# Performance work log

Measured on AMD Instinct MI355X. Metric: run time of the kernel, lower is better.

The kernel has to match this reference:

```python
import jax, jax.numpy as jnp
import numpy as np

B, NA, NB, E = 2, 256, 256, 512
H1, H2 = 300, 100


def setup_inputs() -> dict:
    key = jax.random.key(0)
    ks = jax.random.split(key, 16)

    def n(k, shape, scale=1.0):
        return jax.random.normal(k, shape, dtype=jnp.float32) * scale

    z = lambda shape: jnp.zeros(shape, jnp.float32)
    return {
        "action_embedding": n(ks[0], (B, E, NA)),
        "anchor_embedding": n(ks[1], (B, E, NB)),
        "action_points": n(ks[2], (B, 3, NA)),
        "anchor_points": n(ks[3], (B, 3, NB)),
        # pairwise MLP kernel params: 2E -> 300 -> 100 -> 1
        "mlp_W1": n(ks[4], (2 * E, H1), (2 * E) ** -0.5),
        "mlp_b1": z((H1,)),
        "mlp_W2": n(ks[5], (H1, H2), H1 ** -0.5),
        "mlp_b2": z((H2,)),
        "mlp_W3": n(ks[6], (H2, 1), H2 ** -0.5),
        "mlp_b3": z((1,)),
        # PointNet [512,64,64,64,128,512] (1x1 convs) + Conv1d(512,1,bias=False)
        "pn_W0": n(ks[7], (64, 512), 512 ** -0.5),
        "pn_b0": z((64,)),
        "pn_W1": n(ks[8], (64, 64), 64 ** -0.5),
        "pn_b1": z((64,)),
        "pn_W2": n(ks[9], (64, 64), 64 ** -0.5),
        "pn_b2": z((64,)),
        "pn_W3": n(ks[10], (128, 64), 64 ** -0.5),
        "pn_b3": z((128,)),
        "pn_W4": n(ks[11], (512, 128), 128 ** -0.5),
        "pn_b4": z((512,)),
        "head_W": n(ks[12], (1, 512), 512 ** -0.5),
    }


def reference(action_embedding, anchor_embedding, action_points, anchor_points,
              mlp_W1, mlp_b1, mlp_W2, mlp_b2, mlp_W3, mlp_b3,
              pn_W0, pn_b0, pn_W1, pn_b1, pn_W2, pn_b2, pn_W3, pn_b3,
              pn_W4, pn_b4, head_W):
    P_A = action_points.transpose(0, 2, 1)      # (B, NA, 3)
    P_B = anchor_points.transpose(0, 2, 1)      # (B, NB, 3)
    Phi_A = action_embedding.transpose(0, 2, 1)  # (B, NA, E)
    Phi_B = anchor_embedding.transpose(0, 2, 1)  # (B, NB, E)
    Ed = Phi_A.shape[-1]

    # --- symmetric pairwise MLP kernel: softplus((mlp(cat(a,b)) + mlp(cat(b,a))) / 2) ---
    # First Linear layer is split so the O(NA*NB*2E) concat is never materialized:
    # cat(a,b) @ W1 == a @ W1[:E] + b @ W1[E:]
    W1a, W1b = mlp_W1[:Ed], mlp_W1[Ed:]

    def mlp_tail(h):  # h: (B, NA, NB, H1) pre-activation of layer 1
        h = jax.nn.relu(h)
        h = jax.nn.relu(h @ mlp_W2 + mlp_b2)
        return (h @ mlp_W3 + mlp_b3)[..., 0]  # (B, NA, NB)

    hA_a = Phi_A @ W1a  # (B, NA, H1)
    hA_b = Phi_A @ W1b
    hB_a = Phi_B @ W1a  # (B, NB, H1)
    hB_b = Phi_B @ W1b
    v1 = mlp_tail(hA_a[:, :, None, :] + hB_b[:, None, :, :] + mlp_b1)  # mlp(cat(x1,x2))
    v2 = mlp_tail(hB_a[:, None, :, :] + hA_b[:, :, None, :] + mlp_b1)  # mlp(cat(x2,x1))
    R_est = jax.nn.softplus((v1 + v2) * 0.5)  # (B, NA, NB) estimated distances

    # --- weighted multilateration (estimate_p), vectorized over (B, NA) ---
    # Linearized LS: ||p||^2 - 2 q_k^T p = r_k^2 - ||q_k||^2; subtract weighted means
    # to eliminate ||p||^2, then solve 3x3 weighted normal equations per action point.
    w = jnp.ones(P_B.shape[:2], R_est.dtype)            # (B, NB) uniform weights (last_attn=False)
    wsum = w.sum(-1, keepdims=True)                      # (B, 1)
    qbar = (w[..., None] * P_B).sum(1) / wsum            # (B, 3)
    bvec = (P_B ** 2).sum(-1)[:, None, :] - R_est ** 2   # (B, NA, NB)
    bbar = (w[:, None, :] * bvec).sum(-1) / wsum         # (B, NA)
    Amat = 2.0 * (P_B - qbar[:, None, :])                # (B, NB, 3)
    yvec = bvec - bbar[..., None]                        # (B, NA, NB)
    M = jnp.einsum('bki,bk,bkj->bij', Amat, w, Amat)     # (B, 3, 3)
    rhs = jnp.einsum('bki,bk,bak->bai', Amat, w, yvec)   # (B, NA, 3)
    P_A_B_pred = jnp.linalg.solve(M[:, None], rhs[..., None])[..., 0]  # (B, NA, 3)

    flow = (P_A_B_pred - P_A).transpose(0, 2, 1)         # (B, 3, NA)

    # --- PointNet flow-weight head (1x1 convs + ReLU, final conv no bias) ---
    x = action_embedding                                  # (B, 512, NA)
    for Wc, bc in ((pn_W0, pn_b0), (pn_W1, pn_b1), (pn_W2, pn_b2),
                   (pn_W3, pn_b3), (pn_W4, pn_b4)):
        x = jax.nn.relu(jnp.einsum('oi,bin->bon', Wc, x) + bc[None, :, None])
    weight = jnp.einsum('oi,bin->bon', head_W, x)        # (B, 1, NA)

    full_flow = jnp.concatenate([flow, weight], axis=1)  # (B, 4, NA)
    return full_flow
```

## Files before the change

kernel.cpp:

```cpp
#include <hip/hip_runtime.h>
#include <hip/hip_bf16.h>
#include <hip/hip_fp16.h>

typedef float f32x4 __attribute__((ext_vector_type(4)));
typedef short s16x8 __attribute__((ext_vector_type(8)));
typedef _Float16 f16x8 __attribute__((ext_vector_type(8)));

#define OFF_EMBT   0u
#define OFF_W1T    1048576u
#define OFF_W2TSW  1662976u
#define OFF_W0BF   1734656u
#define OFF_HA     1800192u
#define OFF_R2     3110912u
#define WS_TOTAL   3635200u

__device__ __forceinline__ int pack_bf2(float a, float b) {
  __hip_bfloat162 h = __float22bfloat162_rn(make_float2(a, b));
  int r; __builtin_memcpy(&r, &h, 4); return r;
}
__device__ __forceinline__ unsigned pack_f16_2(float a, float b) {
  __half2 h = __float22half2_rn(make_float2(a, b));
  unsigned r; __builtin_memcpy(&r, &h, 4); return r;
}
__device__ __forceinline__ unsigned short bf16u(float f) {
  __hip_bfloat16 h = __float2bfloat16(f);
  unsigned short u; __builtin_memcpy(&u, &h, 2); return u;
}
__device__ __forceinline__ s16x8 i4_to_s8(int a, int b, int c, int d) {
  union { int i[4]; s16x8 s; } u;
  u.i[0] = a; u.i[1] = b; u.i[2] = c; u.i[3] = d; return u.s;
}

__global__ __launch_bounds__(256) void ka_prep(
    const float* __restrict__ act_emb, const float* __restrict__ anc_emb,
    const float* __restrict__ W1, const float* __restrict__ W2,
    const float* __restrict__ W0pn, char* __restrict__ ws)
{
  __hip_bfloat16* embT  = (__hip_bfloat16*)(ws + OFF_EMBT);
  __hip_bfloat16* W1T   = (__hip_bfloat16*)(ws + OFF_W1T);
  unsigned short* W2Tsw = (unsigned short*)(ws + OFF_W2TSW);
  unsigned short* W0bf  = (unsigned short*)(ws + OFF_W0BF);
  __shared__ float tile[64][65];
  int blk = blockIdx.x, t = threadIdx.x;
  if (blk < 128) {
    int b = blk >> 6, emb = (blk >> 5) & 1, ntile = (blk >> 3) & 3, etile = blk & 7;
    const float* src = emb ? anc_emb : act_emb;
    int e0 = etile * 64, n0 = ntile * 64;
    int rr = t >> 6, cc = t & 63;
    #pragma unroll
    for (int it2 = 0; it2 < 16; ++it2) {
      int e_l = rr * 16 + it2;
      tile[e_l][cc] = src[(size_t)(b * 512 + e0 + e_l) * 256 + n0 + cc];
    }
    __syncthreads();
    int n_l = t >> 2, eq = t & 3;
    unsigned int* dst = (unsigned int*)(embT + ((size_t)((b * 2 + emb) * 256 + n0 + n_l)) * 512 + e0 + eq * 16);
    #pragma unroll
    for (int kk = 0; kk < 8; ++kk)
      dst[kk] = (unsigned)pack_bf2(tile[eq * 16 + 2 * kk][n_l], tile[eq * 16 + 2 * kk + 1][n_l]);
  } else if (blk < 208) {
    int id = blk - 128;
    int half = id / 40; int rem = id % 40; int et = rem / 5; int ct = rem % 5;
    int e0 = et * 64, c0 = ct * 64;
    int rr = t >> 6, cc = t & 63;
    #pragma unroll
    for (int it2 = 0; it2 < 16; ++it2) {
      int e_l = rr * 16 + it2;
      int c = c0 + cc;
      tile[e_l][cc] = (c < 300) ? W1[(size_t)(half * 512 + e0 + e_l) * 300 + c] : 0.f;
    }
    __syncthreads();
    int c_l = t >> 2, eq = t & 3;
    if (c0 + c_l < 300) {
      unsigned int* dst = (unsigned int*)(W1T + ((size_t)(half * 300 + c0 + c_l)) * 512 + e0 + eq * 16);
      #pragma unroll
      for (int kk = 0; kk < 8; ++kk)
        dst[kk] = (unsigned)pack_bf2(tile[eq * 16 + 2 * kk][c_l], tile[eq * 16 + 2 * kk + 1][c_l]);
    }
  } else if (blk < 226) {
    int idx = (blk - 208) * 256 + t;
    if (idx < 4480) {
      int nt = idx / 640; int rem = idx - nt * 640; int ks = rem >> 6; int lane = rem & 63;
      int n = nt * 16 + (lane & 15);
      int kb = ks * 32 + (lane >> 4) * 8;
      unsigned int q[4];
      #pragma unroll
      for (int jj = 0; jj < 4; ++jj) {
        int k0 = kb + jj * 2, k1 = kb + jj * 2 + 1;
        float f0 = (n < 100 && k0 < 300) ? W2[(size_t)k0 * 100 + n] : 0.f;
        float f1 = (n < 100 && k1 < 300) ? W2[(size_t)k1 * 100 + n] : 0.f;
        q[jj] = pack_f16_2(f0, f1);
      }
      ((uint4*)W2Tsw)[idx] = make_uint4(q[0], q[1], q[2], q[3]);
    }
  } else if (blk < 242) {
    int idx = (blk - 226) * 256 + t;
    const float* s = W0pn + (size_t)idx * 8;
    ((uint4*)W0bf)[idx] = make_uint4(
        (unsigned)pack_bf2(s[0], s[1]), (unsigned)pack_bf2(s[2], s[3]),
        (unsigned)pack_bf2(s[4], s[5]), (unsigned)pack_bf2(s[6], s[7]));
  } else {
    int idx = (blk - 242) * 256 + t;
    _Float16* ha = (_Float16*)(ws + OFF_HA);
    #pragma unroll
    for (int rr = 0; rr < 2; ++rr) {
      int row = idx * 2 + rr;
      unsigned* p = (unsigned*)(ha + (size_t)row * 320 + 300);
      #pragma unroll
      for (int q2 = 0; q2 < 10; ++q2) p[q2] = 0u;
    }
  }
}

template<int K, int NT>
__device__ __forceinline__ void pn_layer(unsigned short* xb, const float* __restrict__ W,
                                         const float* __restrict__ bias, int wv, int l, int g)
{
  constexpr int NN = NT / 4;
  f32x4 z = {0.f, 0.f, 0.f, 0.f};
  f32x4 acc[NN];
  #pragma unroll
  for (int nn = 0; nn < NN; ++nn) acc[nn] = z;
  #pragma unroll
  for (int nn = 0; nn < NN; ++nn) {
    int o = (wv + nn * 4) * 16 + l;
    const float* wr0 = W + (size_t)o * K;
    #pragma unroll
    for (int ks = 0; ks < K / 32; ++ks) {
      int koff = ks * 32 + g * 8;
      f32x4 wa = *(const f32x4*)(wr0 + koff);
      f32x4 wb = *(const f32x4*)(wr0 + koff + 4);
      s16x8 bfr = i4_to_s8(pack_bf2(wa.x, wa.y), pack_bf2(wa.z, wa.w),
                           pack_bf2(wb.x, wb.y), pack_bf2(wb.z, wb.w));
      s16x8 a0 = *(const s16x8*)(xb + (size_t)l * 520 + koff);
      acc[nn] = __builtin_amdgcn_mfma_f32_16x16x32_bf16(a0, bfr, acc[nn], 0, 0, 0);
    }
  }
  __syncthreads();
  #pragma unroll
  for (int nn = 0; nn < NN; ++nn) {
    int chan = (wv + nn * 4) * 16 + l;
    float bv = bias[chan];
    #pragma unroll
    for (int r = 0; r < 4; ++r)
      xb[(size_t)(g * 4 + r) * 520 + chan] = bf16u(fmaxf(acc[nn][r] + bv, 0.f));
  }
  __syncthreads();
}

__global__ __launch_bounds__(256) void k1_ha(
    const __hip_bfloat16* __restrict__ embT, const __hip_bfloat16* __restrict__ W1T,
    const float* __restrict__ b1, _Float16* __restrict__ ha_ws,
    const unsigned short* __restrict__ W0bf,
    const float* __restrict__ pnW1, const float* __restrict__ pnW2,
    const float* __restrict__ pnW3, const float* __restrict__ pnW4,
    const float* __restrict__ pnB0, const float* __restrict__ pnB1,
    const float* __restrict__ pnB2, const float* __restrict__ pnB3,
    const float* __restrict__ pnB4,
    const float* __restrict__ headW, float* __restrict__ out)
{
  __shared__ unsigned short xbuf[16 * 520];
  int blk = blockIdx.x, t = threadIdx.x;
  int wv = t >> 6, lane = t & 63, l = lane & 15, g = lane >> 4;
  if (blk < 320) {
    int b = blk / 160; int r = blk % 160; int emb = r / 80; r %= 80;
    int mch = r / 5; int nch = r % 5;
    int m0 = mch * 16;
    const unsigned short* Ap = (const unsigned short*)embT +
        ((size_t)((b * 2 + emb) * 256 + m0 + l)) * 512;
    const unsigned short* Wp = (const unsigned short*)W1T;
    f32x4 z = {0.f, 0.f, 0.f, 0.f};
    f32x4 acc[2] = {z, z};
    for (int ks = 0; ks < 16; ++ks) {
      int k0 = ks * 32 + g * 8;
      s16x8 af = *(const s16x8*)(Ap + k0);
      #pragma unroll
      for (int q = 0; q < 2; ++q) {
        int c = nch * 120 + (wv * 2 + q) * 16 + l;
        s16x8 bf = {0, 0, 0, 0, 0, 0, 0, 0};
        if (c < 600) bf = *(const s16x8*)(Wp + (size_t)c * 512 + k0);
        acc[q] = __builtin_amdgcn_mfma_f32_16x16x32_bf16(af, bf, acc[q], 0, 0, 0);
      }
    }
    #pragma unroll
    for (int q = 0; q < 2; ++q) {
      int cl = (wv * 2 + q) * 16 + l;
      int c = nch * 120 + cl;
      if (cl < 120 && c < 600) {
        int half = (c >= 300) ? 1 : 0;
        int cc = c - half * 300;
        float bias = (emb == 0) ? b1[cc] : 0.f;
        _Float16* Dp = ha_ws + ((size_t)((b * 4 + emb * 2 + half) * 256 + m0 + g * 4)) * 320 + cc;
        #pragma unroll
        for (int r2 = 0; r2 < 4; ++r2)
          Dp[(size_t)r2 * 320] = (_Float16)__float2half_rn(acc[q][r2] + bias);
      }
    }
  } else {
    int pn = blk - 320;
    int b_pn = pn >> 4, n0 = (pn & 15) * 16;
    unsigned short* xb = xbuf;
    {
      const unsigned short* A0 = (const unsigned short*)embT + ((size_t)(b_pn * 2 * 256 + n0)) * 512;
      f32x4 acc0 = {0.f, 0.f, 0.f, 0.f};
      int o = wv * 16 + l;
      const unsigned short* w0r = W0bf + (size_t)o * 512;
      #pragma unroll
      for (int ks = 0; ks < 16; ++ks) {
        int koff = ks * 32 + g * 8;
        s16x8 bfr = *(const s16x8*)(w0r + koff);
        s16x8 a0 = *(const s16x8*)(A0 + (size_t)l * 512 + koff);
        acc0 = __builtin_amdgcn_mfma_f32_16x16x32_bf16(a0, bfr, acc0, 0, 0, 0);
      }
      float bv = pnB0[o];
      #pragma unroll
      for (int r2 = 0; r2 < 4; ++r2)
        xb[(size_t)(g * 4 + r2) * 520 + o] = bf16u(fmaxf(acc0[r2] + bv, 0.f));
      __syncthreads();
    }
    pn_layer<64, 4>(xb, pnW1, pnB1, wv, l, g);
    pn_layer<64, 4>(xb, pnW2, pnB2, wv, l, g);
    pn_layer<64, 8>(xb, pnW3, pnB3, wv, l, g);
    pn_layer<128, 32>(xb, pnW4, pnB4, wv, l, g);
    {
      int p_l = t >> 4, os = t & 15;
      const unsigned short* row = xb + (size_t)p_l * 520 + os * 32;
      float s = 0.f;
      #pragma unroll
      for (int c = 0; c < 32; ++c) {
        unsigned int u = ((unsigned int)row[c]) << 16;
        float xv; __builtin_memcpy(&xv, &u, 4);
        s += xv * headW[os * 32 + c];
      }
      s += __shfl_xor(s, 1); s += __shfl_xor(s, 2);
      s += __shfl_xor(s, 4); s += __shfl_xor(s, 8);
      if (os == 0) out[(size_t)(b_pn * 4 + 3) * 256 + n0 + p_l] = s;
    }
  }
}

__global__ __launch_bounds__(512, 4) void k2_main(
    const _Float16* __restrict__ ha_ws, const unsigned short* __restrict__ W2Tsw,
    const float* __restrict__ b2g, const float* __restrict__ W3g, const float* __restrict__ b3g,
    float* __restrict__ R2)
{
  __shared__ int4 w2s[4480];
  int blk = blockIdx.x, t = threadIdx.x;
  int wv = t >> 6, lane = t & 63, l = lane & 15, g = lane >> 4;
  int b = blk >> 9, it = (blk >> 5) & 15, jt = blk & 31;
  int i0 = it * 16, j = jt * 8 + wv;
  {
    const int4* w2g = (const int4*)W2Tsw;
    for (int u = t; u < 4480; u += 512) w2s[u] = w2g[u];
  }
  __syncthreads();
  const _Float16* hap0 = ha_ws + ((size_t)((b * 4 + 0) * 256 + i0 + l)) * 320;
  const _Float16* hap1 = ha_ws + ((size_t)((b * 4 + 1) * 256 + i0 + l)) * 320;
  const _Float16* hbp0 = ha_ws + ((size_t)((b * 4 + 3) * 256 + j)) * 320;
  const _Float16* hbp1 = ha_ws + ((size_t)((b * 4 + 2) * 256 + j)) * 320;
  f32x4 z = {0.f, 0.f, 0.f, 0.f};
  f32x4 acc0[7], acc1[7];
  #pragma unroll
  for (int nt = 0; nt < 7; ++nt) { acc0[nt] = z; acc1[nt] = z; }
  const f16x8 zf = {0, 0, 0, 0, 0, 0, 0, 0};
  #pragma unroll
  for (int ks = 0; ks < 10; ++ks) {
    int koff = ks * 32 + g * 8;
    f16x8 ha0 = *(const f16x8*)(hap0 + koff);
    f16x8 hb0 = *(const f16x8*)(hbp0 + koff);
    f16x8 ha1 = *(const f16x8*)(hap1 + koff);
    f16x8 hb1 = *(const f16x8*)(hbp1 + koff);
    f16x8 af0 = __builtin_elementwise_max(ha0 + hb0, zf);
    f16x8 af1 = __builtin_elementwise_max(ha1 + hb1, zf);
    #pragma unroll
    for (int nt = 0; nt < 7; ++nt) {
      f16x8 bf = *(const f16x8*)&w2s[(nt * 10 + ks) * 64 + lane];
      acc0[nt] = __builtin_amdgcn_mfma_f32_16x16x32_f16(af0, bf, acc0[nt], 0, 0, 0);
      acc1[nt] = __builtin_amdgcn_mfma_f32_16x16x32_f16(af1, bf, acc1[nt], 0, 0, 0);
    }
  }
  {
    float w3v[7], b2v[7];
    #pragma unroll
    for (int nt = 0; nt < 7; ++nt) {
      int n = nt * 16 + l;
      w3v[nt] = (n < 100) ? W3g[n] : 0.f;
      b2v[nt] = (n < 100) ? b2g[n] : 0.f;
    }
    float b3 = b3g[0];
    #pragma unroll
    for (int r = 0; r < 4; ++r) {
      float pv = 0.f;
      #pragma unroll
      for (int nt = 0; nt < 7; ++nt) {
        pv += fmaxf(acc0[nt][r] + b2v[nt], 0.f) * w3v[nt];
        pv += fmaxf(acc1[nt][r] + b2v[nt], 0.f) * w3v[nt];
      }
      pv += __shfl_xor(pv, 1);
      pv += __shfl_xor(pv, 2);
      pv += __shfl_xor(pv, 4);
      pv += __shfl_xor(pv, 8);
      float S = 0.5f * pv + b3;
      float Rr = (S > 20.f) ? S : log1pf(expf(S));
      if (l == 0)
        R2[((size_t)(b * 256 + i0 + g * 4 + r)) * 256 + j] = Rr * Rr;
    }
  }
}

__device__ __forceinline__ float block_sum(float v, float* redbuf, int t) {
  #pragma unroll
  for (int m = 1; m < 64; m <<= 1) v += __shfl_xor(v, m);
  __syncthreads();
  if ((t & 63) == 0) redbuf[t >> 6] = v;
  __syncthreads();
  return redbuf[0] + redbuf[1] + redbuf[2] + redbuf[3];
}

__global__ __launch_bounds__(256) void k3_solve(
    const float* __restrict__ anc_pts, const float* __restrict__ act_pts,
    const float* __restrict__ R2, float* __restrict__ out)
{
  __shared__ float Ax[256], Ay[256], Az[256];
  __shared__ float redbuf[4];
  int blk = blockIdx.x, t = threadIdx.x;
  int b = blk >> 2, ic = blk & 3;
  int k = t;
  float px = anc_pts[(size_t)(b * 3 + 0) * 256 + k];
  float py = anc_pts[(size_t)(b * 3 + 1) * 256 + k];
  float pz = anc_pts[(size_t)(b * 3 + 2) * 256 + k];
  float qx = block_sum(px, redbuf, t) * (1.f / 256.f);
  float qy = block_sum(py, redbuf, t) * (1.f / 256.f);
  float qz = block_sum(pz, redbuf, t) * (1.f / 256.f);
  float ax = 2.f * (px - qx), ay = 2.f * (py - qy), az = 2.f * (pz - qz);
  float p2 = px * px + py * py + pz * pz;
  Ax[k] = ax; Ay[k] = ay; Az[k] = az;
  float mxx = block_sum(ax * ax, redbuf, t);
  float mxy = block_sum(ax * ay, redbuf, t);
  float mxz = block_sum(ax * az, redbuf, t);
  float myy = block_sum(ay * ay, redbuf, t);
  float myz = block_sum(ay * az, redbuf, t);
  float mzz = block_sum(az * az, redbuf, t);
  float c0x = block_sum(ax * p2, redbuf, t);
  float c0y = block_sum(ay * p2, redbuf, t);
  float c0z = block_sum(az * p2, redbuf, t);
  __syncthreads();
  float det = mxx * (myy * mzz - myz * myz) - mxy * (mxy * mzz - myz * mxz) + mxz * (mxy * myz - myy * mxz);
  float idet = 1.f / det;
  float i00 = (myy * mzz - myz * myz) * idet;
  float i01 = (mxz * myz - mxy * mzz) * idet;
  float i02 = (mxy * myz - mxz * myy) * idet;
  float i11 = (mxx * mzz - mxz * mxz) * idet;
  float i12 = (mxy * mxz - mxx * myz) * idet;
  float i22 = (mxx * myy - mxy * mxy) * idet;
  int il = t >> 2, ks = t & 3;
  int i = ic * 64 + il;
  const float* rrow = R2 + ((size_t)(b * 256 + i)) * 256;
  float r0 = 0.f, r1 = 0.f, r2 = 0.f;
  #pragma unroll
  for (int kk = 0; kk < 16; ++kk) {
    int kb = ks * 64 + kk * 4;
    f32x4 rv = *(const f32x4*)(rrow + kb);
    r0 += Ax[kb] * rv.x + Ax[kb + 1] * rv.y + Ax[kb + 2] * rv.z + Ax[kb + 3] * rv.w;
    r1 += Ay[kb] * rv.x + Ay[kb + 1] * rv.y + Ay[kb + 2] * rv.z + Ay[kb + 3] * rv.w;
    r2 += Az[kb] * rv.x + Az[kb + 1] * rv.y + Az[kb + 2] * rv.z + Az[kb + 3] * rv.w;
  }
  r0 += __shfl_xor(r0, 1); r0 += __shfl_xor(r0, 2);
  r1 += __shfl_xor(r1, 1); r1 += __shfl_xor(r1, 2);
  r2 += __shfl_xor(r2, 1); r2 += __shfl_xor(r2, 2);
  if (ks == 0) {
    float hx = c0x - r0, hy = c0y - r1, hz = c0z - r2;
    float x0 = i00 * hx + i01 * hy + i02 * hz;
    float x1 = i01 * hx + i11 * hy + i12 * hz;
    float x2 = i02 * hx + i12 * hy + i22 * hz;
    out[(size_t)(b * 4 + 0) * 256 + i] = x0 - act_pts[(size_t)(b * 3 + 0) * 256 + i];
    out[(size_t)(b * 4 + 1) * 256 + i] = x1 - act_pts[(size_t)(b * 3 + 1) * 256 + i];
    out[(size_t)(b * 4 + 2) * 256 + i] = x2 - act_pts[(size_t)(b * 3 + 2) * 256 + i];
  }
}

extern "C" void kernel_launch(void* const* d_in, const int* in_sizes, int n_in,
                              void* d_out, int out_size, void* d_ws, size_t ws_size,
                              hipStream_t stream)
{
  const float* act_emb = (const float*)d_in[0];
  const float* anc_emb = (const float*)d_in[1];
  const float* act_pts = (const float*)d_in[2];
  const float* anc_pts = (const float*)d_in[3];
  const float* W1  = (const float*)d_in[4];
  const float* b1  = (const float*)d_in[5];
  const float* W2  = (const float*)d_in[6];
  const float* b2  = (const float*)d_in[7];
  const float* W3  = (const float*)d_in[8];
  const float* b3  = (const float*)d_in[9];
  const float* pnW0 = (const float*)d_in[10];
  const float* pnB0 = (const float*)d_in[11];
  const float* pnW1 = (const float*)d_in[12];
  const float* pnB1 = (const float*)d_in[13];
  const float* pnW2 = (const float*)d_in[14];
  const float* pnB2 = (const float*)d_in[15];
  const float* pnW3 = (const float*)d_in[16];
  const float* pnB3 = (const float*)d_in[17];
  const float* pnW4 = (const float*)d_in[18];
  const float* pnB4 = (const float*)d_in[19];
  const float* headW = (const float*)d_in[20];
  char* ws = (char*)d_ws;
  __hip_bfloat16* embT  = (__hip_bfloat16*)(ws + OFF_EMBT);
  __hip_bfloat16* W1T   = (__hip_bfloat16*)(ws + OFF_W1T);
  unsigned short* W2Tsw = (unsigned short*)(ws + OFF_W2TSW);
  unsigned short* W0bf  = (unsigned short*)(ws + OFF_W0BF);
  _Float16* ha_ws = (_Float16*)(ws + OFF_HA);
  float* R2ws  = (float*)(ws + OFF_R2);
  float* outp  = (float*)d_out;

  ka_prep<<<246, 256, 0, stream>>>(act_emb, anc_emb, W1, W2, pnW0, ws);
  k1_ha<<<352, 256, 0, stream>>>(embT, W1T, b1, ha_ws, W0bf,
                                 pnW1, pnW2, pnW3, pnW4, pnB0, pnB1, pnB2, pnB3, pnB4,
                                 headW, outp);
  k2_main<<<1024, 512, 0, stream>>>(ha_ws, W2Tsw, b2, W3, b3, R2ws);
  k3_solve<<<8, 256, 0, stream>>>(anc_pts, act_pts, R2ws, outp);
}
```

Before: 168.2 us.

## Split symmetric MLP halves across wave groups in 1024-thread blocks

The pairwise MLP kernel now runs 1024 threads per block. Each half of the waves computes one ordering of the symmetric pair (a,b or b,a), where before a single wave computed both. Partial sums are combined through shared memory after an extra barrier. The W2 swizzle layout is reordered so the seven n-tiles of each k-step sit contiguously, which simplifies LDS addressing. This halves per-wave accumulator registers and doubles wave parallelism, at the cost of an extra sync and LDS exchange, and a large block that may limit occupancy.

```diff
diff --git a/kernel.cpp b/kernel.cpp
--- a/kernel.cpp
+++ b/kernel.cpp
@@ -80,7 +80,8 @@
   } else if (blk < 226) {
     int idx = (blk - 208) * 256 + t;
     if (idx < 4480) {
-      int nt = idx / 640; int rem = idx - nt * 640; int ks = rem >> 6; int lane = rem & 63;
+      int unit = idx >> 6; int lane = idx & 63;
+      int ks = unit / 7; int nt = unit - ks * 7;
       int n = nt * 16 + (lane & 15);
       int kb = ks * 32 + (lane >> 4) * 8;
       unsigned int q[4];
@@ -239,46 +240,43 @@
   }
 }
 
-__global__ __launch_bounds__(512, 4) void k2_main(
+__global__ __launch_bounds__(1024, 8) void k2_main(
     const _Float16* __restrict__ ha_ws, const unsigned short* __restrict__ W2Tsw,
     const float* __restrict__ b2g, const float* __restrict__ W3g, const float* __restrict__ b3g,
     float* __restrict__ R2)
 {
   __shared__ int4 w2s[4480];
+  __shared__ float pvbuf[128];
   int blk = blockIdx.x, t = threadIdx.x;
   int wv = t >> 6, lane = t & 63, l = lane & 15, g = lane >> 4;
+  int rep = wv >> 3, jw = wv & 7;
   int b = blk >> 9, it = (blk >> 5) & 15, jt = blk & 31;
-  int i0 = it * 16, j = jt * 8 + wv;
+  int i0 = it * 16, j = jt * 8 + jw;
   {
     const int4* w2g = (const int4*)W2Tsw;
-    for (int u = t; u < 4480; u += 512) w2s[u] = w2g[u];
-  }
-  __syncthreads();
-  const _Float16* hap0 = ha_ws + ((size_t)((b * 4 + 0) * 256 + i0 + l)) * 320;
-  const _Float16* hap1 = ha_ws + ((size_t)((b * 4 + 1) * 256 + i0 + l)) * 320;
-  const _Float16* hbp0 = ha_ws + ((size_t)((b * 4 + 3) * 256 + j)) * 320;
-  const _Float16* hbp1 = ha_ws + ((size_t)((b * 4 + 2) * 256 + j)) * 320;
+    for (int u = t; u < 4480; u += 1024) w2s[u] = w2g[u];
+  }
+  __syncthreads();
+  const _Float16* hap = ha_ws + ((size_t)((b * 4 + rep) * 256 + i0 + l)) * 320 + g * 8;
+  const _Float16* hbp = ha_ws + ((size_t)((b * 4 + (rep ? 2 : 3)) * 256 + j)) * 320 + g * 8;
   f32x4 z = {0.f, 0.f, 0.f, 0.f};
-  f32x4 acc0[7], acc1[7];
-  #pragma unroll
-  for (int nt = 0; nt < 7; ++nt) { acc0[nt] = z; acc1[nt] = z; }
+  f32x4 acc[7];
+  #pragma unroll
+  for (int nt = 0; nt < 7; ++nt) acc[nt] = z;
   const f16x8 zf = {0, 0, 0, 0, 0, 0, 0, 0};
   #pragma unroll
   for (int ks = 0; ks < 10; ++ks) {
-    int koff = ks * 32 + g * 8;
-    f16x8 ha0 = *(const f16x8*)(hap0 + koff);
-    f16x8 hb0 = *(const f16x8*)(hbp0 + koff);
-    f16x8 ha1 = *(const f16x8*)(hap1 + koff);
-    f16x8 hb1 = *(const f16x8*)(hbp1 + koff);
-    f16x8 af0 = __builtin_elementwise_max(ha0 + hb0, zf);
-    f16x8 af1 = __builtin_elementwise_max(ha1 + hb1, zf);
+    f16x8 ha = *(const f16x8*)(hap + ks * 32);
+    f16x8 hb = *(const f16x8*)(hbp + ks * 32);
+    f16x8 af = __builtin_elementwise_max(ha + hb, zf);
+    const int4* wp = &w2s[ks * 448 + lane];
     #pragma unroll
     for (int nt = 0; nt < 7; ++nt) {
-      f16x8 bf = *(const f16x8*)&w2s[(nt * 10 + ks) * 64 + lane];
-      acc0[nt] = __builtin_amdgcn_mfma_f32_16x16x32_f16(af0, bf, acc0[nt], 0, 0, 0);
-      acc1[nt] = __builtin_amdgcn_mfma_f32_16x16x32_f16(af1, bf, acc1[nt], 0, 0, 0);
-    }
-  }
+      f16x8 bf = *(const f16x8*)(wp + nt * 64);
+      acc[nt] = __builtin_amdgcn_mfma_f32_16x16x32_f16(af, bf, acc[nt], 0, 0, 0);
+    }
+  }
+  float pv[4];
   {
     float w3v[7], b2v[7];
     #pragma unroll
@@ -287,23 +285,31 @@
       w3v[nt] = (n < 100) ? W3g[n] : 0.f;
       b2v[nt] = (n < 100) ? b2g[n] : 0.f;
     }
+    #pragma unroll
+    for (int r = 0; r < 4; ++r) {
+      float p = 0.f;
+      #pragma unroll
+      for (int nt = 0; nt < 7; ++nt)
+        p += fmaxf(acc[nt][r] + b2v[nt], 0.f) * w3v[nt];
+      p += __shfl_xor(p, 1);
+      p += __shfl_xor(p, 2);
+      p += __shfl_xor(p, 4);
+      p += __shfl_xor(p, 8);
+      pv[r] = p;
+    }
+  }
+  if (rep == 1 && l == 0) {
+    #pragma unroll
+    for (int r = 0; r < 4; ++r) pvbuf[jw * 16 + g * 4 + r] = pv[r];
+  }
+  __syncthreads();
+  if (rep == 0 && l == 0) {
     float b3 = b3g[0];
     #pragma unroll
     for (int r = 0; r < 4; ++r) {
-      float pv = 0.f;
-      #pragma unroll
-      for (int nt = 0; nt < 7; ++nt) {
-        pv += fmaxf(acc0[nt][r] + b2v[nt], 0.f) * w3v[nt];
-        pv += fmaxf(acc1[nt][r] + b2v[nt], 0.f) * w3v[nt];
-      }
-      pv += __shfl_xor(pv, 1);
-      pv += __shfl_xor(pv, 2);
-      pv += __shfl_xor(pv, 4);
-      pv += __shfl_xor(pv, 8);
-      float S = 0.5f * pv + b3;
+      float S = 0.5f * (pv[r] + pvbuf[jw * 16 + g * 4 + r]) + b3;
       float Rr = (S > 20.f) ? S : log1pf(expf(S));
-      if (l == 0)
-        R2[((size_t)(b * 256 + i0 + g * 4 + r)) * 256 + j] = Rr * Rr;
+      R2[((size_t)(b * 256 + i0 + g * 4 + r)) * 256 + j] = Rr * Rr;
     }
   }
 }
@@ -417,6 +423,6 @@
   k1_ha<<<352, 256, 0, stream>>>(embT, W1T, b1, ha_ws, W0bf,
                                  pnW1, pnW2, pnW3, pnW4, pnB0, pnB1, pnB2, pnB3, pnB4,
                                  headW, outp);
-  k2_main<<<1024, 512, 0, stream>>>(ha_ws, W2Tsw, b2, W3, b3, R2ws);
+  k2_main<<<1024, 1024, 0, stream>>>(ha_ws, W2Tsw, b2, W3, b3, R2ws);
   k3_solve<<<8, 256, 0, stream>>>(anc_pts, act_pts, R2ws, outp);
 }
```

New measurement: 168.8 us. Within noise of the previous version (+0.4%).
